# Kernel tuning notes

Measured on AMD Instinct MI355X. Metric: run time of the kernel, lower is better.

The kernel has to match this reference:

```python
import jax, jax.numpy as jnp
import numpy as np

N_NODES = 50000
N_EDGES = 500000
D = 128
BN_EPS = 1e-5
AGG_EPS = 1e-6


def _batch_norm(x, gamma, beta):
    # training-mode BatchNorm1d: normalize over the batch (row) axis with biased variance
    mean = jnp.mean(x, axis=0)
    var = jnp.var(x, axis=0)
    return (x - mean) * jax.lax.rsqrt(var + BN_EPS) * gamma + beta


def setup_inputs() -> dict:
    key = jax.random.key(0)
    ks = jax.random.split(key, 10)
    w_scale = 1.0 / np.sqrt(D)
    inp = {
        "h": jax.random.normal(ks[0], (N_NODES, D), dtype=jnp.float32),
        "e": jax.random.normal(ks[1], (N_EDGES, D), dtype=jnp.float32),
        "src": jax.random.randint(ks[2], (N_EDGES,), 0, N_NODES),
        "dst": jax.random.randint(ks[3], (N_EDGES,), 0, N_NODES),
    }
    for i, name in enumerate(["A", "B", "C", "D", "E"]):
        inp[f"W_{name}"] = jax.random.normal(ks[4 + i], (D, D), dtype=jnp.float32) * w_scale
        inp[f"b_{name}"] = jnp.zeros((D,), dtype=jnp.float32)
    inp["gamma_h"] = jnp.ones((D,), dtype=jnp.float32)
    inp["beta_h"] = jnp.zeros((D,), dtype=jnp.float32)
    inp["gamma_e"] = jnp.ones((D,), dtype=jnp.float32)
    inp["beta_e"] = jnp.zeros((D,), dtype=jnp.float32)
    return inp


def reference(h, e, src, dst, W_A, b_A, W_B, b_B, W_C, b_C, W_D, b_D, W_E, b_E,
              gamma_h, beta_h, gamma_e, beta_e):
    n = h.shape[0]
    # node projections
    Ah = h @ W_A.T + b_A
    Bh = h @ W_B.T + b_B
    Dh = h @ W_D.T + b_D
    Eh = h @ W_E.T + b_E
    Ce = e @ W_C.T + b_C
    # edge update: u_add_v(Dh, Eh) + Ce
    e_new = Dh[src] + Eh[dst] + Ce            # [E, D]
    sigma = jax.nn.sigmoid(e_new)              # [E, D]
    # gated aggregation to destination nodes
    sum_sigma_h = jax.ops.segment_sum(Bh[src] * sigma, dst, num_segments=n)
    sum_sigma = jax.ops.segment_sum(sigma, dst, num_segments=n)
    h_new = Ah + sum_sigma_h / (sum_sigma + AGG_EPS)
    # batch norm (training-mode) + relu + residual; dropout p=0.0 -> identity
    h_out = jax.nn.relu(_batch_norm(h_new, gamma_h, beta_h))
    e_out = jax.nn.relu(_batch_norm(e_new, gamma_e, beta_e))
    h_out = h + h_out
    e_out = e + e_out
    return h_out, e_out
```

## Files before the change

kernel.cpp:

```cpp
#include <hip/hip_runtime.h>
#include <hip/hip_bf16.h>


#define NN 50000
#define NE 500000
#define DD 128

typedef __attribute__((ext_vector_type(8))) short short8;
typedef __attribute__((ext_vector_type(4))) float floatx4;

__device__ inline short f2bf(float f) {
    unsigned u = __builtin_bit_cast(unsigned, f);
    u += 0x7FFFu + ((u >> 16) & 1u);
    return (short)(u >> 16);
}

__device__ inline short8 load_frag(const float* __restrict__ p) {
    float4 a = *(const float4*)p;
    float4 b = *(const float4*)(p + 4);
    short8 r;
    r[0] = f2bf(a.x); r[1] = f2bf(a.y); r[2] = f2bf(a.z); r[3] = f2bf(a.w);
    r[4] = f2bf(b.x); r[5] = f2bf(b.y); r[6] = f2bf(b.z); r[7] = f2bf(b.w);
    return r;
}

__device__ inline void stage_W(const float* __restrict__ W, short* Wlds) {
    int t = threadIdx.x;
    int r = t >> 1;
    int half = t & 1;
#pragma unroll
    for (int k = 0; k < 8; k++) {
        int sub = half * 8 + k;
        const float* p = W + (size_t)r * DD + sub * 8;
        float4 a = *(const float4*)p;
        float4 b = *(const float4*)(p + 4);
        short8 v;
        v[0] = f2bf(a.x); v[1] = f2bf(a.y); v[2] = f2bf(a.z); v[3] = f2bf(a.w);
        v[4] = f2bf(b.x); v[5] = f2bf(b.y); v[6] = f2bf(b.z); v[7] = f2bf(b.w);
        int slot = r * 16 + (sub ^ (r & 15));
        *(short8*)&Wlds[slot * 8] = v;
    }
}

__launch_bounds__(256, 2)
__global__ void node_gemm(const float* __restrict__ h,
                          const float* W0, const float* W1, const float* W2, const float* W3,
                          const float* b0, const float* b1, const float* b2, const float* b3,
                          float* o0, float* o1, float* o2, float* o3) {
    __shared__ short Wlds[DD * DD];
    int mtx = blockIdx.y;
    const float* W = (mtx == 0) ? W0 : (mtx == 1) ? W1 : (mtx == 2) ? W2 : W3;
    const float* bias_p = (mtx == 0) ? b0 : (mtx == 1) ? b1 : (mtx == 2) ? b2 : b3;
    float* out = (mtx == 0) ? o0 : (mtx == 1) ? o1 : (mtx == 2) ? o2 : o3;

    stage_W(W, Wlds);

    int lane = threadIdx.x & 63;
    int wid = threadIdx.x >> 6;
    int m = lane & 15, quad = lane >> 4;
    int gw = blockIdx.x * 4 + wid;
    int nw = gridDim.x * 4;

    float bias[8];
#pragma unroll
    for (int tn = 0; tn < 8; tn++) bias[tn] = bias_p[tn * 16 + m];

    int wbase[4];
#pragma unroll
    for (int c = 0; c < 4; c++)
        wbase[c] = (m * 16 + ((c * 4 + quad) ^ m)) * 16;

    __syncthreads();

    const int NT = NN / 16;
    for (int t = gw; t < NT; t += nw) {
        int rowb = t * 16;
        short8 af[4];
#pragma unroll
        for (int c = 0; c < 4; c++)
            af[c] = load_frag(h + (size_t)(rowb + m) * DD + c * 32 + quad * 8);
        floatx4 acc[8];
#pragma unroll
        for (int tn = 0; tn < 8; tn++) acc[tn] = (floatx4)bias[tn];
#pragma unroll
        for (int tn = 0; tn < 8; tn++) {
#pragma unroll
            for (int c = 0; c < 4; c++) {
                short8 wfr = *(const short8*)((const char*)Wlds + (wbase[c] + tn * 4096));
                acc[tn] = __builtin_amdgcn_mfma_f32_16x16x32_bf16(af[c], wfr, acc[tn], 0, 0, 0);
            }
        }
        int r0 = rowb + quad * 4;
#pragma unroll
        for (int r = 0; r < 4; r++) {
            float* op = out + (size_t)(r0 + r) * DD;
#pragma unroll
            for (int tn = 0; tn < 8; tn++) {
                int col = tn * 16 + m;
                op[col] = acc[tn][r];
            }
        }
    }
}

__launch_bounds__(256, 2)
__global__ void edge_gemm(const float* __restrict__ e,
                          const float* __restrict__ Wc, const float* __restrict__ bc,
                          const float* __restrict__ Dh, const float* __restrict__ Eh,
                          const int* __restrict__ src, const int* __restrict__ dst,
                          float* __restrict__ enew,
                          float* __restrict__ cs_e, float* __restrict__ cq_e) {
    __shared__ short Wlds[DD * DD];
    stage_W(Wc, Wlds);

    int lane = threadIdx.x & 63;
    int wid = threadIdx.x >> 6;
    int m = lane & 15, quad = lane >> 4;
    int gw = blockIdx.x * 4 + wid;
    int nw = gridDim.x * 4;

    float bias[8];
#pragma unroll
    for (int tn = 0; tn < 8; tn++) bias[tn] = bc[tn * 16 + m];

    int wbase[4];
#pragma unroll
    for (int c = 0; c < 4; c++)
        wbase[c] = (m * 16 + ((c * 4 + quad) ^ m)) * 16;

    __syncthreads();

    float ssum[8] = {};
    float ssq[8] = {};

    const int NT = NE / 16;
    for (int t = gw; t < NT; t += nw) {
        int rowb = t * 16;
        short8 af[4];
#pragma unroll
        for (int c = 0; c < 4; c++)
            af[c] = load_frag(e + (size_t)(rowb + m) * DD + c * 32 + quad * 8);
        floatx4 acc[8];
#pragma unroll
        for (int tn = 0; tn < 8; tn++) acc[tn] = (floatx4)bias[tn];
#pragma unroll
        for (int tn = 0; tn < 8; tn++) {
#pragma unroll
            for (int c = 0; c < 4; c++) {
                short8 wfr = *(const short8*)((const char*)Wlds + (wbase[c] + tn * 4096));
                acc[tn] = __builtin_amdgcn_mfma_f32_16x16x32_bf16(af[c], wfr, acc[tn], 0, 0, 0);
            }
        }

        int e0 = rowb + quad * 4;
        int4 s4 = *(const int4*)(src + e0);
        int4 d4 = *(const int4*)(dst + e0);
        int sarr[4] = {s4.x, s4.y, s4.z, s4.w};
        int darr[4] = {d4.x, d4.y, d4.z, d4.w};
#pragma unroll
        for (int r = 0; r < 4; r++) {
            const float* dp = Dh + (size_t)sarr[r] * DD;
            const float* ep = Eh + (size_t)darr[r] * DD;
            float* op = enew + (size_t)(e0 + r) * DD;
#pragma unroll
            for (int tn = 0; tn < 8; tn++) {
                int col = tn * 16 + m;
                float v = acc[tn][r] + dp[col] + ep[col];
                op[col] = v;
                ssum[tn] += v;
                ssq[tn] += v * v;
            }
        }
    }

#pragma unroll
    for (int tn = 0; tn < 8; tn++) {
        float s = ssum[tn], q = ssq[tn];
        s += __shfl_xor(s, 32); s += __shfl_xor(s, 16);
        q += __shfl_xor(q, 32); q += __shfl_xor(q, 16);
        if (quad == 0) {
            atomicAdd(&cs_e[tn * 16 + m], s);
            atomicAdd(&cq_e[tn * 16 + m], q);
        }
    }
}

__global__ void hist_kernel(const int* __restrict__ dst, int* __restrict__ counts) {
    int i = blockIdx.x * blockDim.x + threadIdx.x;
    if (i < NE) atomicAdd(&counts[dst[i]], 1);
}

__global__ void scan_kernel(const int* __restrict__ counts,
                            int* __restrict__ rowptr, int* __restrict__ cursor) {
    __shared__ int lds[1024];
    int t = threadIdx.x;
    const int CH = (NN + 1023) / 1024;
    int begin = t * CH;
    int end = begin + CH; if (end > NN) end = NN; if (begin > NN) begin = NN;
    int s = 0;
    for (int i = begin; i < end; i++) s += counts[i];
    lds[t] = s;
    __syncthreads();
    for (int off = 1; off < 1024; off <<= 1) {
        int v = lds[t];
        int add = (t >= off) ? lds[t - off] : 0;
        __syncthreads();
        lds[t] = v + add;
        __syncthreads();
    }
    int run = (t == 0) ? 0 : lds[t - 1];
    for (int i = begin; i < end; i++) {
        rowptr[i] = run; cursor[i] = run;
        run += counts[i];
    }
    if (t == 1023) rowptr[NN] = run;
}

__global__ void scatter_kernel(const int* __restrict__ src, const int* __restrict__ dst,
                               int* __restrict__ cursor,
                               int* __restrict__ eidx, int* __restrict__ ssrc) {
    int i = blockIdx.x * blockDim.x + threadIdx.x;
    if (i < NE) {
        int d = dst[i];
        int pos = atomicAdd(&cursor[d], 1);
        eidx[pos] = i;
        ssrc[pos] = src[i];
    }
}

__launch_bounds__(256)
__global__ void aggregate(const int* __restrict__ rowptr, const int* __restrict__ eidx,
                          const int* __restrict__ ssrc,
                          const float* __restrict__ enew, const float* __restrict__ Bh,
                          const float* __restrict__ Ah, float* __restrict__ hnew) {
    int gw = (blockIdx.x * blockDim.x + threadIdx.x) >> 6;
    int lane = threadIdx.x & 63;
    if (gw >= NN) return;
    int s = rowptr[gw], e = rowptr[gw + 1];
    int c0 = lane * 2;
    float a1x = 0.f, a1y = 0.f, a2x = 0.f, a2y = 0.f;
    float2 xv = {0.f, 0.f}, bv = {0.f, 0.f};
    if (s < e) {
        int eid = eidx[s], sr = ssrc[s];
        xv = *(const float2*)(enew + (size_t)eid * DD + c0);
        bv = *(const float2*)(Bh + (size_t)sr * DD + c0);
    }
    for (int j = s; j < e; j++) {
        float2 x = xv, b = bv;
        if (j + 1 < e) {
            int eid2 = eidx[j + 1], sr2 = ssrc[j + 1];
            xv = *(const float2*)(enew + (size_t)eid2 * DD + c0);
            bv = *(const float2*)(Bh + (size_t)sr2 * DD + c0);
        }
        float sx = 1.f / (1.f + __expf(-x.x));
        float sy = 1.f / (1.f + __expf(-x.y));
        a1x = fmaf(sx, b.x, a1x); a1y = fmaf(sy, b.y, a1y);
        a2x += sx; a2y += sy;
    }
    float2 ah = *(const float2*)(Ah + (size_t)gw * DD + c0);
    float2 o;
    o.x = ah.x + a1x / (a2x + 1e-6f);
    o.y = ah.y + a1y / (a2y + 1e-6f);
    *(float2*)(hnew + (size_t)gw * DD + c0) = o;
}

__global__ void hstats(const float* __restrict__ hnew, float* __restrict__ cs, float* __restrict__ cq) {
    int d = threadIdx.x;
    float s = 0.f, q = 0.f;
    for (int v = blockIdx.x; v < NN; v += gridDim.x) {
        float x = hnew[(size_t)v * DD + d];
        s += x; q += x * x;
    }
    atomicAdd(&cs[d], s);
    atomicAdd(&cq[d], q);
}

__global__ void finalize(const float* cs_e, const float* cq_e,
                         const float* cs_h, const float* cq_h,
                         const float* ge, const float* be,
                         const float* gh, const float* bh,
                         float* mul_e, float* add_e, float* mul_h, float* add_h) {
    int d = threadIdx.x;
    float me = cs_e[d] / (float)NE;
    float ve = cq_e[d] / (float)NE - me * me;
    float se = rsqrtf(ve + 1e-5f) * ge[d];
    mul_e[d] = se; add_e[d] = be[d] - me * se;
    float mh = cs_h[d] / (float)NN;
    float vh = cq_h[d] / (float)NN - mh * mh;
    float sh = rsqrtf(vh + 1e-5f) * gh[d];
    mul_h[d] = sh; add_h[d] = bh[d] - mh * sh;
}

__global__ void out_transform(float* __restrict__ x, const float* __restrict__ orig,
                              const float* __restrict__ mul, const float* __restrict__ add,
                              int total4) {
    int i = blockIdx.x * blockDim.x + threadIdx.x;
    if (i >= total4) return;
    float4 xv = ((const float4*)x)[i];
    float4 ov = ((const float4*)orig)[i];
    int col = (i * 4) & (DD - 1);
    float4 mu = *(const float4*)(mul + col);
    float4 ad = *(const float4*)(add + col);
    float4 y;
    y.x = fmaxf(fmaf(xv.x, mu.x, ad.x), 0.f) + ov.x;
    y.y = fmaxf(fmaf(xv.y, mu.y, ad.y), 0.f) + ov.y;
    y.z = fmaxf(fmaf(xv.z, mu.z, ad.z), 0.f) + ov.z;
    y.w = fmaxf(fmaf(xv.w, mu.w, ad.w), 0.f) + ov.w;
    ((float4*)x)[i] = y;
}

extern "C" void kernel_launch(void* const* d_in, const int* in_sizes, int n_in,
                              void* d_out, int out_size, void* d_ws, size_t ws_size,
                              hipStream_t stream) {
    const float* h   = (const float*)d_in[0];
    const float* e   = (const float*)d_in[1];
    const int*   src = (const int*)d_in[2];
    const int*   dst = (const int*)d_in[3];
    const float* W_A = (const float*)d_in[4];  const float* b_A = (const float*)d_in[5];
    const float* W_B = (const float*)d_in[6];  const float* b_B = (const float*)d_in[7];
    const float* W_C = (const float*)d_in[8];  const float* b_C = (const float*)d_in[9];
    const float* W_D = (const float*)d_in[10]; const float* b_D = (const float*)d_in[11];
    const float* W_E = (const float*)d_in[12]; const float* b_E = (const float*)d_in[13];
    const float* gamma_h = (const float*)d_in[14]; const float* beta_h = (const float*)d_in[15];
    const float* gamma_e = (const float*)d_in[16]; const float* beta_e = (const float*)d_in[17];

    float* out_h = (float*)d_out;
    float* out_e = out_h + (size_t)NN * DD;

    char* ws = (char*)d_ws;
    float* Ah = (float*)(ws + 0);
    float* Bh = (float*)(ws + 25600000);
    float* Dh = (float*)(ws + 51200000);
    float* Eh = (float*)(ws + 76800000);
    int* rowptr = (int*)(ws + 102400000);
    int* counts = (int*)(ws + 102600192);
    int* cursor = (int*)(ws + 102800192);
    int* eidx   = (int*)(ws + 103000192);
    int* ssrc   = (int*)(ws + 105000192);
    float* stats = (float*)(ws + 107000192);
    float* cs_e = stats + 0 * DD;
    float* cq_e = stats + 1 * DD;
    float* cs_h = stats + 2 * DD;
    float* cq_h = stats + 3 * DD;
    float* mul_e = stats + 4 * DD;
    float* add_e = stats + 5 * DD;
    float* mul_h = stats + 6 * DD;
    float* add_h = stats + 7 * DD;

    hipMemsetAsync(counts, 0, NN * sizeof(int), stream);
    hipMemsetAsync(stats, 0, 4 * DD * sizeof(float), stream);

    node_gemm<<<dim3(256, 4), 256, 0, stream>>>(h, W_A, W_B, W_D, W_E,
                                                b_A, b_B, b_D, b_E,
                                                Ah, Bh, Dh, Eh);

    int nb_edge = (NE + 255) / 256;
    hist_kernel<<<nb_edge, 256, 0, stream>>>(dst, counts);
    scan_kernel<<<1, 1024, 0, stream>>>(counts, rowptr, cursor);
    scatter_kernel<<<nb_edge, 256, 0, stream>>>(src, dst, cursor, eidx, ssrc);

    edge_gemm<<<768, 256, 0, stream>>>(e, W_C, b_C, Dh, Eh, src, dst,
                                       out_e, cs_e, cq_e);

    aggregate<<<(NN * 64 + 255) / 256, 256, 0, stream>>>(rowptr, eidx, ssrc, out_e, Bh, Ah, out_h);

    hstats<<<256, DD, 0, stream>>>(out_h, cs_h, cq_h);

    finalize<<<1, DD, 0, stream>>>(cs_e, cq_e, cs_h, cq_h,
                                   gamma_e, beta_e, gamma_h, beta_h,
                                   mul_e, add_e, mul_h, add_h);

    out_transform<<<(NN * DD / 4 + 255) / 256, 256, 0, stream>>>(out_h, h, mul_h, add_h, NN * DD / 4);
    out_transform<<<(NE * DD / 4 + 255) / 256, 256, 0, stream>>>(out_e, e, mul_e, add_e, NE * DD / 4);
}
```

Baseline: 1.134 ms.

## Fuse edge batch-norm output into aggregation and prefetch edge indices

Result: no change. 1.142 ms (+0.7%).

```diff
diff --git a/kernel.cpp b/kernel.cpp
--- a/kernel.cpp
+++ b/kernel.cpp
@@ -134,7 +134,21 @@
     float ssq[8] = {};
 
     const int NT = NE / 16;
+
+    int4 s4 = {0, 0, 0, 0}, d4 = {0, 0, 0, 0};
+    if (gw < NT) {
+        s4 = *(const int4*)(src + gw * 16 + quad * 4);
+        d4 = *(const int4*)(dst + gw * 16 + quad * 4);
+    }
+
     for (int t = gw; t < NT; t += nw) {
+        int4 cs4 = s4, cd4 = d4;
+        int tnext = t + nw;
+        if (tnext < NT) {
+            s4 = *(const int4*)(src + tnext * 16 + quad * 4);
+            d4 = *(const int4*)(dst + tnext * 16 + quad * 4);
+        }
+
         int rowb = t * 16;
         short8 af[4];
 #pragma unroll
@@ -153,10 +167,8 @@
         }
 
         int e0 = rowb + quad * 4;
-        int4 s4 = *(const int4*)(src + e0);
-        int4 d4 = *(const int4*)(dst + e0);
-        int sarr[4] = {s4.x, s4.y, s4.z, s4.w};
-        int darr[4] = {d4.x, d4.y, d4.z, d4.w};
+        int sarr[4] = {cs4.x, cs4.y, cs4.z, cs4.w};
+        int darr[4] = {cd4.x, cd4.y, cd4.z, cd4.w};
 #pragma unroll
         for (int r = 0; r < 4; r++) {
             const float* dp = Dh + (size_t)sarr[r] * DD;
@@ -228,34 +240,70 @@
     }
 }
 
+__global__ void finalize_e(const float* cs, const float* cq,
+                           const float* g, const float* b,
+                           float* mul, float* add) {
+    int d = threadIdx.x;
+    float me = cs[d] / (float)NE;
+    float ve = cq[d] / (float)NE - me * me;
+    float se = rsqrtf(ve + 1e-5f) * g[d];
+    mul[d] = se; add[d] = b[d] - me * se;
+}
+
+__global__ void finalize_h(const float* cs, const float* cq,
+                           const float* g, const float* b,
+                           float* mul, float* add) {
+    int d = threadIdx.x;
+    float mh = cs[d] / (float)NN;
+    float vh = cq[d] / (float)NN - mh * mh;
+    float sh = rsqrtf(vh + 1e-5f) * g[d];
+    mul[d] = sh; add[d] = b[d] - mh * sh;
+}
+
 __launch_bounds__(256)
 __global__ void aggregate(const int* __restrict__ rowptr, const int* __restrict__ eidx,
                           const int* __restrict__ ssrc,
-                          const float* __restrict__ enew, const float* __restrict__ Bh,
-                          const float* __restrict__ Ah, float* __restrict__ hnew) {
+                          float* __restrict__ enew,
+                          const float* __restrict__ eorig,
+                          const float* __restrict__ Bh,
+                          const float* __restrict__ Ah,
+                          const float* __restrict__ mul_e, const float* __restrict__ add_e,
+                          float* __restrict__ hnew) {
     int gw = (blockIdx.x * blockDim.x + threadIdx.x) >> 6;
     int lane = threadIdx.x & 63;
     if (gw >= NN) return;
     int s = rowptr[gw], e = rowptr[gw + 1];
     int c0 = lane * 2;
+    float2 mu = *(const float2*)(mul_e + c0);
+    float2 ad = *(const float2*)(add_e + c0);
     float a1x = 0.f, a1y = 0.f, a2x = 0.f, a2y = 0.f;
-    float2 xv = {0.f, 0.f}, bv = {0.f, 0.f};
+    float2 xv = {0.f, 0.f}, bv = {0.f, 0.f}, ev = {0.f, 0.f};
+    int eid_c = 0;
     if (s < e) {
-        int eid = eidx[s], sr = ssrc[s];
-        xv = *(const float2*)(enew + (size_t)eid * DD + c0);
+        eid_c = eidx[s];
+        int sr = ssrc[s];
+        xv = *(const float2*)(enew + (size_t)eid_c * DD + c0);
         bv = *(const float2*)(Bh + (size_t)sr * DD + c0);
+        ev = *(const float2*)(eorig + (size_t)eid_c * DD + c0);
     }
     for (int j = s; j < e; j++) {
-        float2 x = xv, b = bv;
+        float2 x = xv, b = bv, eo = ev;
+        int eid = eid_c;
         if (j + 1 < e) {
-            int eid2 = eidx[j + 1], sr2 = ssrc[j + 1];
-            xv = *(const float2*)(enew + (size_t)eid2 * DD + c0);
+            eid_c = eidx[j + 1];
+            int sr2 = ssrc[j + 1];
+            xv = *(const float2*)(enew + (size_t)eid_c * DD + c0);
             bv = *(const float2*)(Bh + (size_t)sr2 * DD + c0);
+            ev = *(const float2*)(eorig + (size_t)eid_c * DD + c0);
         }
         float sx = 1.f / (1.f + __expf(-x.x));
         float sy = 1.f / (1.f + __expf(-x.y));
         a1x = fmaf(sx, b.x, a1x); a1y = fmaf(sy, b.y, a1y);
         a2x += sx; a2y += sy;
+        float2 y;
+        y.x = eo.x + fmaxf(fmaf(x.x, mu.x, ad.x), 0.f);
+        y.y = eo.y + fmaxf(fmaf(x.y, mu.y, ad.y), 0.f);
+        *(float2*)(enew + (size_t)eid * DD + c0) = y;
     }
     float2 ah = *(const float2*)(Ah + (size_t)gw * DD + c0);
     float2 o;
@@ -273,22 +321,6 @@
     }
     atomicAdd(&cs[d], s);
     atomicAdd(&cq[d], q);
-}
-
-__global__ void finalize(const float* cs_e, const float* cq_e,
-                         const float* cs_h, const float* cq_h,
-                         const float* ge, const float* be,
-                         const float* gh, const float* bh,
-                         float* mul_e, float* add_e, float* mul_h, float* add_h) {
-    int d = threadIdx.x;
-    float me = cs_e[d] / (float)NE;
-    float ve = cq_e[d] / (float)NE - me * me;
-    float se = rsqrtf(ve + 1e-5f) * ge[d];
-    mul_e[d] = se; add_e[d] = be[d] - me * se;
-    float mh = cs_h[d] / (float)NN;
-    float vh = cq_h[d] / (float)NN - mh * mh;
-    float sh = rsqrtf(vh + 1e-5f) * gh[d];
-    mul_h[d] = sh; add_h[d] = bh[d] - mh * sh;
 }
 
 __global__ void out_transform(float* __restrict__ x, const float* __restrict__ orig,
@@ -359,17 +391,18 @@
     scan_kernel<<<1, 1024, 0, stream>>>(counts, rowptr, cursor);
     scatter_kernel<<<nb_edge, 256, 0, stream>>>(src, dst, cursor, eidx, ssrc);
 
-    edge_gemm<<<768, 256, 0, stream>>>(e, W_C, b_C, Dh, Eh, src, dst,
-                                       out_e, cs_e, cq_e);
-
-    aggregate<<<(NN * 64 + 255) / 256, 256, 0, stream>>>(rowptr, eidx, ssrc, out_e, Bh, Ah, out_h);
+    edge_gemm<<<1024, 256, 0, stream>>>(e, W_C, b_C, Dh, Eh, src, dst,
+                                        out_e, cs_e, cq_e);
+
+    finalize_e<<<1, DD, 0, stream>>>(cs_e, cq_e, gamma_e, beta_e, mul_e, add_e);
+
+    aggregate<<<(NN * 64 + 255) / 256, 256, 0, stream>>>(rowptr, eidx, ssrc,
+                                                         out_e, e, Bh, Ah,
+                                                         mul_e, add_e, out_h);
 
     hstats<<<256, DD, 0, stream>>>(out_h, cs_h, cq_h);
 
-    finalize<<<1, DD, 0, stream>>>(cs_e, cq_e, cs_h, cq_h,
-                                   gamma_e, beta_e, gamma_h, beta_h,
-                                   mul_e, add_e, mul_h, add_h);
+    finalize_h<<<1, DD, 0, stream>>>(cs_h, cq_h, gamma_h, beta_h, mul_h, add_h);
 
     out_transform<<<(NN * DD / 4 + 255) / 256, 256, 0, stream>>>(out_h, h, mul_h, add_h, NN * DD / 4);
-    out_transform<<<(NE * DD / 4 + 255) / 256, 256, 0, stream>>>(out_e, e, mul_e, add_e, NE * DD / 4);
-}
+}
```
